# Kernel tuning notes

Hardware: AMD Instinct MI355X
Metric: run time of the kernel (lower is better)

The kernel has to match this reference:

```python
import jax, jax.numpy as jnp
import numpy as np

N = 100000
E = 1600000
IN_DIM = 128
HID = 64


def setup_inputs() -> dict:
    key = jax.random.key(0)
    ks = jax.random.split(key, 10)
    x = jax.random.normal(ks[0], (N, IN_DIM), dtype=jnp.float32)
    edge_index = jax.random.randint(ks[1], (2, E), 0, N, dtype=jnp.int32)
    s1 = 1.0 / np.sqrt(IN_DIM)
    s2 = 1.0 / np.sqrt(HID)
    return {
        "x": x,
        "edge_index": edge_index,
        "W1_l": jax.random.uniform(ks[2], (IN_DIM, HID), jnp.float32, -s1, s1),
        "W1_r": jax.random.uniform(ks[3], (IN_DIM, HID), jnp.float32, -s1, s1),
        "b1": jnp.zeros((HID,), jnp.float32),
        "W2_l": jax.random.uniform(ks[4], (HID, HID), jnp.float32, -s2, s2),
        "W2_r": jax.random.uniform(ks[5], (HID, HID), jnp.float32, -s2, s2),
        "b2": jnp.zeros((HID,), jnp.float32),
        "Wc": jax.random.uniform(ks[6], (HID, 1), jnp.float32, -s2, s2),
        "bc": jnp.zeros((1,), jnp.float32),
    }


def _sage_conv(x, src, dst, inv_deg, W_l, W_r, b):
    # mean-aggregate neighbor features: gather x[src], scatter-sum into dst
    msg = x[src]  # [E, d] irregular gather
    agg = jax.ops.segment_sum(msg, dst, num_segments=N) * inv_deg  # [N, d]
    return agg @ W_l + x @ W_r + b


def reference(x, edge_index, W1_l, W1_r, b1, W2_l, W2_r, b2, Wc, bc):
    src, dst = edge_index[0], edge_index[1]
    deg = jax.ops.segment_sum(jnp.ones((E,), jnp.float32), dst, num_segments=N)
    inv_deg = (1.0 / jnp.maximum(deg, 1.0))[:, None]  # [N,1]
    h = jax.nn.relu(_sage_conv(x, src, dst, inv_deg, W1_l, W1_r, b1))
    # dropout is identity at inference
    h = jax.nn.relu(_sage_conv(h, src, dst, inv_deg, W2_l, W2_r, b2))
    return h @ Wc + bc  # [N, 1] raw logits
```

## Files before the change

### kernel.cpp

```cpp
#include <hip/hip_runtime.h>
#include <hip/hip_bf16.h>

#define N_NODES 100000
#define N_EDGES 1600000
#define IN_DIM  128
#define HID     64

#define PSTRIDE 48
#define NBKT      391
#define BCAP2     4608
#define PREA_BLKS 400
#define EPBA      (N_EDGES / PREA_BLKS)
#define PREP_BLKS 12
#define PRE_BLKS  (PREA_BLKS + PREP_BLKS)
#define GEMM1_BLKS 782

typedef __attribute__((ext_vector_type(8))) short bf16x8;
typedef __attribute__((ext_vector_type(4))) float f32x4;
typedef __attribute__((ext_vector_type(8))) float f32x8;
typedef __attribute__((ext_vector_type(2))) float f32x2;
typedef __attribute__((ext_vector_type(4))) int   i32x4;

__device__ inline unsigned short f2bf_u(float x) {
    __hip_bfloat16 h = __float2bfloat16(x);
    return __builtin_bit_cast(unsigned short, h);
}
__device__ inline float bfu2f(unsigned short u) {
    unsigned v = ((unsigned)u) << 16;
    return __builtin_bit_cast(float, v);
}
__device__ inline unsigned char f2fp8(float x) {
    unsigned e = (unsigned)__builtin_amdgcn_cvt_pk_fp8_f32(x, x, 0, false);
    return (unsigned char)(e & 0xff);
}
__device__ inline void acc_fp8x8(f32x8& acc, uint2 m) {
    f32x2 p0 = __builtin_amdgcn_cvt_pk_f32_fp8(m.x, false);
    f32x2 p1 = __builtin_amdgcn_cvt_pk_f32_fp8(m.x, true);
    f32x2 p2 = __builtin_amdgcn_cvt_pk_f32_fp8(m.y, false);
    f32x2 p3 = __builtin_amdgcn_cvt_pk_f32_fp8(m.y, true);
    acc[0] += p0[0]; acc[1] += p0[1];
    acc[2] += p1[0]; acc[3] += p1[1];
    acc[4] += p2[0]; acc[5] += p2[1];
    acc[6] += p3[0]; acc[7] += p3[1];
}
__device__ inline void acc_bf16x8(f32x8& acc, bf16x8 m) {
#pragma unroll
    for (int q = 0; q < 8; ++q) acc[q] += bfu2f((unsigned short)m[q]);
}

__device__ inline void prep_pack(const float* __restrict__ Wl,
                                 const float* __restrict__ Wr,
                                 ushort2* __restrict__ Bhi,
                                 ushort2* __restrict__ Blo, int idx) {
    int j  = idx & 3;
    int l  = (idx >> 2) & 63;
    int c  = (idx >> 8) & 7;
    int kt = idx >> 11;
    int col = c * 16 + (l & 15);
    int k0  = kt * 32 + (l >> 4) * 8 + 2 * j;
    const float* W = (col < 64) ? Wl : Wr;
    int cc = col & 63;
    float w0 = W[(size_t)k0 * 64 + cc];
    float w1 = W[(size_t)(k0 + 1) * 64 + cc];
    unsigned short h0 = f2bf_u(w0), h1 = f2bf_u(w1);
    unsigned short lo0 = f2bf_u(w0 - bfu2f(h0)), lo1 = f2bf_u(w1 - bfu2f(h1));
    Bhi[idx] = make_ushort2(h0, h1);
    Blo[idx] = make_ushort2(lo0, lo1);
}

__global__ __launch_bounds__(1024) void k_pre(const int* __restrict__ ei,
                                              int* __restrict__ gcnt,
                                              uint2* __restrict__ ebuf,
                                              const float* __restrict__ W1l,
                                              const float* __restrict__ W1r,
                                              const float* __restrict__ W2l,
                                              const float* __restrict__ W2r,
                                              ushort2* __restrict__ Bh1,
                                              ushort2* __restrict__ Bl1,
                                              ushort2* __restrict__ Bh2,
                                              ushort2* __restrict__ Bl2) {
    const int tid = threadIdx.x;
    if (blockIdx.x >= PREA_BLKS) {
        int idx = (blockIdx.x - PREA_BLKS) * 1024 + tid;
        if (idx < 8192)       prep_pack(W1l, W1r, Bh1, Bl1, idx);
        else if (idx < 12288) prep_pack(W2l, W2r, Bh2, Bl2, idx - 8192);
        return;
    }
    __shared__ int hist[NBKT], gbase[NBKT];
    for (int i = tid; i < NBKT; i += 1024) hist[i] = 0;
    __syncthreads();
    const int start = blockIdx.x * EPBA;
    const int end   = start + EPBA;
    const int* __restrict__ src = ei;
    const int* __restrict__ dst = ei + N_EDGES;
    for (int i = start + tid; i < end; i += 1024)
        atomicAdd(&hist[dst[i] >> 8], 1);
    __syncthreads();
    for (int i = tid; i < NBKT; i += 1024) {
        int h = hist[i];
        gbase[i] = (h > 0) ? atomicAdd(&gcnt[i], h) : 0;
        hist[i] = 0;
    }
    __syncthreads();
    for (int i = start + tid; i < end; i += 1024) {
        int d = dst[i];
        int s = src[i];
        int b = d >> 8;
        int r = gbase[b] + atomicAdd(&hist[b], 1);
        if (r < BCAP2) ebuf[(size_t)b * BCAP2 + r] = make_uint2((unsigned)d, (unsigned)s);
    }
}

__global__ __launch_bounds__(256) void k_preB(const int* __restrict__ gcnt,
                                              const uint2* __restrict__ ebuf,
                                              int* __restrict__ adj,
                                              int* __restrict__ deg) {
    __shared__ int adjL[256 * PSTRIDE];
    __shared__ int degL[256];
    const int b   = blockIdx.x;
    const int tid = threadIdx.x;
    degL[tid] = 0;
    {
        i32x4* z4 = (i32x4*)adjL;
        for (int i = tid; i < 256 * PSTRIDE / 4; i += 256) z4[i] = (i32x4)(0);
    }
    __syncthreads();
    const int cnt  = min(gcnt[b], BCAP2);
    const int base = b << 8;
    const uint2* __restrict__ eb = ebuf + (size_t)b * BCAP2;
    for (int i = tid; i < cnt; i += 256) {
        uint2 p = eb[i];
        int r = (int)p.x - base;
        int pos = atomicAdd(&degL[r], 1);
        if (pos < PSTRIDE) adjL[r * PSTRIDE + pos] = (int)p.y;
    }
    __syncthreads();
    const int node = base + tid;
    if (node < N_NODES) deg[node] = degL[tid];
    i32x4* __restrict__ dstp = (i32x4*)(adj + (size_t)base * PSTRIDE);
    const i32x4* __restrict__ srcp = (const i32x4*)adjL;
    for (int i = tid; i < 256 * PSTRIDE / 4; i += 256)
        dstp[i] = srcp[i];
}

__global__ __launch_bounds__(256) void k_gemm1(const float* __restrict__ X,
                                               const i32x4* __restrict__ Bhi,
                                               const i32x4* __restrict__ Blo,
                                               const float* __restrict__ bias,
                                               unsigned char* __restrict__ Yf8,
                                               unsigned short* __restrict__ Dbf, int n) {
    const int K = IN_DIM;
    const int lane = threadIdx.x & 63;
    const int wid  = threadIdx.x >> 6;
    const int m0   = (blockIdx.x * 4 + wid) * 32;
    if (m0 >= n) return;
    const int r  = lane & 15;
    const int kg = lane >> 4;

    f32x4 acc[2][8];
#pragma unroll
    for (int mt = 0; mt < 2; ++mt)
#pragma unroll
        for (int c = 0; c < 8; ++c) acc[mt][c] = (f32x4)(0.f);

#pragma unroll
    for (int kt = 0; kt < K / 32; ++kt) {
        bf16x8 ah[2];
#pragma unroll
        for (int mt = 0; mt < 2; ++mt) {
            const f32x4* p = (const f32x4*)(X + (size_t)(m0 + mt * 16 + r) * K + kt * 32 + kg * 8);
            f32x4 x0 = __builtin_nontemporal_load(p);
            f32x4 x1 = __builtin_nontemporal_load(p + 1);
#pragma unroll
            for (int t = 0; t < 4; ++t) {
                ah[mt][t]     = (short)f2bf_u(x0[t]);
                ah[mt][4 + t] = (short)f2bf_u(x1[t]);
            }
        }
#pragma unroll
        for (int c = 0; c < 8; ++c) {
            const int bi = (kt * 8 + c) * 64 + lane;
            bf16x8 bh = __builtin_bit_cast(bf16x8, Bhi[bi]);
            bf16x8 bl = __builtin_bit_cast(bf16x8, Blo[bi]);
#pragma unroll
            for (int mt = 0; mt < 2; ++mt) {
                acc[mt][c] = __builtin_amdgcn_mfma_f32_16x16x32_bf16(ah[mt], bh, acc[mt][c], 0, 0, 0);
                acc[mt][c] = __builtin_amdgcn_mfma_f32_16x16x32_bf16(ah[mt], bl, acc[mt][c], 0, 0, 0);
            }
        }
    }
#pragma unroll
    for (int mt = 0; mt < 2; ++mt) {
#pragma unroll
        for (int c = 0; c < 8; ++c) {
            int col = c * 16 + r;
            float badd = (c >= 4) ? bias[col - 64] : 0.f;
#pragma unroll
            for (int j = 0; j < 4; ++j) {
                int row = m0 + mt * 16 + kg * 4 + j;
                if (row < n) {
                    if (c < 4) Yf8[(size_t)row * 64 + col] = f2fp8(acc[mt][c][j]);
                    else       Dbf[(size_t)row * 64 + col - 64] = f2bf_u(acc[mt][c][j] + badd);
                }
            }
        }
    }
}

__global__ __launch_bounds__(256) void k_agg1f(const unsigned char* __restrict__ Af8,
                                               unsigned short* __restrict__ Dbf,
                                               const int* __restrict__ adj,
                                               const int* __restrict__ deg,
                                               const i32x4* __restrict__ Bhi,
                                               const i32x4* __restrict__ Blo,
                                               const float* __restrict__ bias,
                                               unsigned short* __restrict__ Bbf) {
    __shared__ unsigned short hs[32][72];
    __shared__ int adjL[32][PSTRIDE];
    __shared__ int degL[32];
    const int tid  = threadIdx.x;
    const int lane = tid & 63;
    const int wv   = tid >> 6;
    const int v0   = blockIdx.x * 32;
    {
        const int* asrc = adj + (size_t)v0 * PSTRIDE;
        for (int i = tid; i < 32 * PSTRIDE; i += 256) ((int*)adjL)[i] = asrc[i];
        if (tid < 32) degL[tid] = deg[v0 + tid];
    }
    __syncthreads();
    const int t  = lane >> 3;
    const int c  = lane & 7;
    const int nt = wv * 8 + t;
    const int v  = v0 + nt;
    const int dgf = degL[nt];
    const int d = min(dgf, PSTRIDE);
    const float iv = 1.0f / (float)max(dgf, 1);
    const uint2* __restrict__ A2 = (const uint2*)Af8;
    f32x8 acc = (f32x8)(0.f);
    int i = 0;
    for (; i + 4 <= d; i += 4) {
        int u0 = adjL[nt][i], u1 = adjL[nt][i + 1], u2 = adjL[nt][i + 2], u3 = adjL[nt][i + 3];
        uint2 m0 = A2[(size_t)u0 * 8 + c];
        uint2 m1 = A2[(size_t)u1 * 8 + c];
        uint2 m2 = A2[(size_t)u2 * 8 + c];
        uint2 m3 = A2[(size_t)u3 * 8 + c];
        acc_fp8x8(acc, m0); acc_fp8x8(acc, m1); acc_fp8x8(acc, m2); acc_fp8x8(acc, m3);
    }
    for (; i < d; ++i) {
        int u0 = adjL[nt][i];
        uint2 m0 = A2[(size_t)u0 * 8 + c];
        acc_fp8x8(acc, m0);
    }
    {
        bf16x8 zb = ((const bf16x8*)Dbf)[(size_t)v * 8 + c];
        bf16x8 hb;
#pragma unroll
        for (int q = 0; q < 8; ++q)
            hb[q] = (short)f2bf_u(fmaxf(fmaf(acc[q], iv, bfu2f((unsigned short)zb[q])), 0.f));
        *(bf16x8*)&hs[nt][c * 8] = hb;
    }
    __syncthreads();
    const int r  = lane & 15;
    const int kg = lane >> 4;
    f32x4 acc2[2][2];
#pragma unroll
    for (int mt = 0; mt < 2; ++mt)
#pragma unroll
        for (int ci = 0; ci < 2; ++ci) acc2[mt][ci] = (f32x4)(0.f);
#pragma unroll
    for (int kt = 0; kt < 2; ++kt) {
        bf16x8 ah[2];
#pragma unroll
        for (int mt = 0; mt < 2; ++mt)
            ah[mt] = *(const bf16x8*)&hs[mt * 16 + r][kt * 32 + kg * 8];
#pragma unroll
        for (int ci = 0; ci < 2; ++ci) {
            const int cg = wv * 2 + ci;
            const int bi = (kt * 8 + cg) * 64 + lane;
            bf16x8 bh = __builtin_bit_cast(bf16x8, Bhi[bi]);
            bf16x8 bl = __builtin_bit_cast(bf16x8, Blo[bi]);
#pragma unroll
            for (int mt = 0; mt < 2; ++mt) {
                acc2[mt][ci] = __builtin_amdgcn_mfma_f32_16x16x32_bf16(ah[mt], bh, acc2[mt][ci], 0, 0, 0);
                acc2[mt][ci] = __builtin_amdgcn_mfma_f32_16x16x32_bf16(ah[mt], bl, acc2[mt][ci], 0, 0, 0);
            }
        }
    }
#pragma unroll
    for (int mt = 0; mt < 2; ++mt) {
#pragma unroll
        for (int ci = 0; ci < 2; ++ci) {
            const int cg = wv * 2 + ci;
            const int col = cg * 16 + r;
            const float badd = (cg >= 4) ? bias[col - 64] : 0.f;
#pragma unroll
            for (int jj = 0; jj < 4; ++jj) {
                const int row = v0 + mt * 16 + kg * 4 + jj;
                if (cg < 4) Bbf[(size_t)row * 64 + col] = f2bf_u(acc2[mt][ci][jj]);
                else        Dbf[(size_t)row * 64 + col - 64] = f2bf_u(acc2[mt][ci][jj] + badd);
            }
        }
    }
}

__global__ __launch_bounds__(256) void k_agg2(const unsigned short* __restrict__ Abf,
                                              const unsigned short* __restrict__ Zbf,
                                              const int* __restrict__ adj,
                                              const int* __restrict__ deg,
                                              const float* __restrict__ Wc,
                                              const float* __restrict__ bc,
                                              float* __restrict__ out, int n) {
    __shared__ int adjL[32][PSTRIDE];
    __shared__ int degL[32];
    const int tid  = threadIdx.x;
    const int lane = tid & 63;
    const int wv   = tid >> 6;
    const int v0   = blockIdx.x * 32;
    {
        const int* asrc = adj + (size_t)v0 * PSTRIDE;
        for (int i = tid; i < 32 * PSTRIDE; i += 256) ((int*)adjL)[i] = asrc[i];
        if (tid < 32) degL[tid] = deg[v0 + tid];
    }
    __syncthreads();
    const int t  = lane >> 3;
    const int c  = lane & 7;
    const int nt = wv * 8 + t;
    const int v  = v0 + nt;
    const int dgf = degL[nt];
    const int d = min(dgf, PSTRIDE);
    const float iv = 1.0f / (float)max(dgf, 1);
    const bf16x8* __restrict__ A8 = (const bf16x8*)Abf;
    f32x8 acc = (f32x8)(0.f);
    int i = 0;
    for (; i + 4 <= d; i += 4) {
        int u0 = adjL[nt][i], u1 = adjL[nt][i + 1], u2 = adjL[nt][i + 2], u3 = adjL[nt][i + 3];
        bf16x8 m0 = A8[(size_t)u0 * 8 + c];
        bf16x8 m1 = A8[(size_t)u1 * 8 + c];
        bf16x8 m2 = A8[(size_t)u2 * 8 + c];
        bf16x8 m3 = A8[(size_t)u3 * 8 + c];
        acc_bf16x8(acc, m0); acc_bf16x8(acc, m1); acc_bf16x8(acc, m2); acc_bf16x8(acc, m3);
    }
    for (; i < d; ++i) {
        int u0 = adjL[nt][i];
        bf16x8 m0 = A8[(size_t)u0 * 8 + c];
        acc_bf16x8(acc, m0);
    }
    bf16x8 zb = ((const bf16x8*)Zbf)[(size_t)v * 8 + c];
    const float4* Wc4 = (const float4*)Wc;
    float4 w0 = Wc4[c * 2], w1 = Wc4[c * 2 + 1];
    float h;
    float pv = 0.f;
    h = fmaxf(fmaf(acc[0], iv, bfu2f((unsigned short)zb[0])), 0.f); pv += h * w0.x;
    h = fmaxf(fmaf(acc[1], iv, bfu2f((unsigned short)zb[1])), 0.f); pv += h * w0.y;
    h = fmaxf(fmaf(acc[2], iv, bfu2f((unsigned short)zb[2])), 0.f); pv += h * w0.z;
    h = fmaxf(fmaf(acc[3], iv, bfu2f((unsigned short)zb[3])), 0.f); pv += h * w0.w;
    h = fmaxf(fmaf(acc[4], iv, bfu2f((unsigned short)zb[4])), 0.f); pv += h * w1.x;
    h = fmaxf(fmaf(acc[5], iv, bfu2f((unsigned short)zb[5])), 0.f); pv += h * w1.y;
    h = fmaxf(fmaf(acc[6], iv, bfu2f((unsigned short)zb[6])), 0.f); pv += h * w1.z;
    h = fmaxf(fmaf(acc[7], iv, bfu2f((unsigned short)zb[7])), 0.f); pv += h * w1.w;
    pv += __shfl_xor(pv, 1, 64);
    pv += __shfl_xor(pv, 2, 64);
    pv += __shfl_xor(pv, 4, 64);
    if (c == 0 && v < n) out[v] = pv + bc[0];
}

extern "C" void kernel_launch(void* const* d_in, const int* in_sizes, int n_in,
                              void* d_out, int out_size, void* d_ws, size_t ws_size,
                              hipStream_t stream) {
    const float* x   = (const float*)d_in[0];
    const int*   ei  = (const int*)d_in[1];
    const float* W1l = (const float*)d_in[2];
    const float* W1r = (const float*)d_in[3];
    const float* b1  = (const float*)d_in[4];
    const float* W2l = (const float*)d_in[5];
    const float* W2r = (const float*)d_in[6];
    const float* b2  = (const float*)d_in[7];
    const float* Wc  = (const float*)d_in[8];
    const float* bc  = (const float*)d_in[9];
    float* out = (float*)d_out;

    char* w = (char*)d_ws;
    auto carve = [&](size_t bytes) -> void* {
        void* p = (void*)w;
        w += (bytes + 255) & ~(size_t)255;
        return p;
    };
    int* gcnt = (int*)carve((size_t)NBKT * 4);
    int* deg  = (int*)carve((size_t)N_NODES * 4);
    int* adj  = (int*)carve((size_t)(N_NODES + 256) * PSTRIDE * 4);
    unsigned char*  Af8 = (unsigned char*)carve((size_t)N_NODES * HID);
    unsigned short* Bbf = (unsigned short*)carve((size_t)N_NODES * HID * 2);
    unsigned short* Dbf = (unsigned short*)carve((size_t)N_NODES * HID * 2);
    uint2* ebuf = (uint2*)carve((size_t)NBKT * BCAP2 * 8);
    ushort2* Bh1 = (ushort2*)carve((size_t)(IN_DIM / 32) * 8 * 64 * 4 * 4);
    ushort2* Bl1 = (ushort2*)carve((size_t)(IN_DIM / 32) * 8 * 64 * 4 * 4);
    ushort2* Bh2 = (ushort2*)carve((size_t)(HID / 32) * 8 * 64 * 4 * 4);
    ushort2* Bl2 = (ushort2*)carve((size_t)(HID / 32) * 8 * 64 * 4 * 4);

    hipMemsetAsync(gcnt, 0, (size_t)NBKT * 4, stream);

    k_pre<<<PRE_BLKS, 1024, 0, stream>>>(ei, gcnt, ebuf, W1l, W1r, W2l, W2r, Bh1, Bl1, Bh2, Bl2);
    k_preB<<<NBKT, 256, 0, stream>>>(gcnt, ebuf, adj, deg);
    k_gemm1<<<GEMM1_BLKS, 256, 0, stream>>>(x, (const i32x4*)Bh1, (const i32x4*)Bl1, b1, Af8, Dbf, N_NODES);
    k_agg1f<<<N_NODES / 32, 256, 0, stream>>>(Af8, Dbf, adj, deg,
                                              (const i32x4*)Bh2, (const i32x4*)Bl2, b2, Bbf);
    k_agg2<<<N_NODES / 32, 256, 0, stream>>>(Bbf, Dbf, adj, deg, Wc, bc, out, N_NODES);
}
```

Measured before the change: 136.8 us.

## Store layer-2 gather table as fp8 and unroll neighbor gathers by eight

The layer-2 projected neighbor features written by the first aggregation kernel are now stored as fp8 instead of bf16, and the second aggregation gathers them with fp8 unpacking. This halves the bytes moved by the irregular per-edge gather. Both aggregation loops also issue eight independent gathers per iteration to raise memory-level parallelism. The shared adjacency tile is padded to 49 ints per row to avoid LDS bank conflicts. The fp8 storage adds quantization error to the second layer's aggregated messages.

```diff
diff --git a/kernel.cpp b/kernel.cpp
--- a/kernel.cpp
+++ b/kernel.cpp
@@ -7,6 +7,7 @@
 #define HID     64
 
 #define PSTRIDE 48
+#define PADJ    49
 #define NBKT      391
 #define BCAP2     4608
 #define PREA_BLKS 400
@@ -42,10 +43,6 @@
     acc[2] += p1[0]; acc[3] += p1[1];
     acc[4] += p2[0]; acc[5] += p2[1];
     acc[6] += p3[0]; acc[7] += p3[1];
-}
-__device__ inline void acc_bf16x8(f32x8& acc, bf16x8 m) {
-#pragma unroll
-    for (int q = 0; q < 8; ++q) acc[q] += bfu2f((unsigned short)m[q]);
 }
 
 __device__ inline void prep_pack(const float* __restrict__ Wl,
@@ -214,9 +211,9 @@
                                                const i32x4* __restrict__ Bhi,
                                                const i32x4* __restrict__ Blo,
                                                const float* __restrict__ bias,
-                                               unsigned short* __restrict__ Bbf) {
+                                               unsigned char* __restrict__ Bf8) {
     __shared__ unsigned short hs[32][72];
-    __shared__ int adjL[32][PSTRIDE];
+    __shared__ int adjL[32][PADJ];
     __shared__ int degL[32];
     const int tid  = threadIdx.x;
     const int lane = tid & 63;
@@ -224,7 +221,8 @@
     const int v0   = blockIdx.x * 32;
     {
         const int* asrc = adj + (size_t)v0 * PSTRIDE;
-        for (int i = tid; i < 32 * PSTRIDE; i += 256) ((int*)adjL)[i] = asrc[i];
+        for (int i = tid; i < 32 * PSTRIDE; i += 256)
+            adjL[i / PSTRIDE][i % PSTRIDE] = asrc[i];
         if (tid < 32) degL[tid] = deg[v0 + tid];
     }
     __syncthreads();
@@ -238,6 +236,20 @@
     const uint2* __restrict__ A2 = (const uint2*)Af8;
     f32x8 acc = (f32x8)(0.f);
     int i = 0;
+    for (; i + 8 <= d; i += 8) {
+        int u0 = adjL[nt][i],     u1 = adjL[nt][i + 1], u2 = adjL[nt][i + 2], u3 = adjL[nt][i + 3];
+        int u4 = adjL[nt][i + 4], u5 = adjL[nt][i + 5], u6 = adjL[nt][i + 6], u7 = adjL[nt][i + 7];
+        uint2 m0 = A2[(size_t)u0 * 8 + c];
+        uint2 m1 = A2[(size_t)u1 * 8 + c];
+        uint2 m2 = A2[(size_t)u2 * 8 + c];
+        uint2 m3 = A2[(size_t)u3 * 8 + c];
+        uint2 m4 = A2[(size_t)u4 * 8 + c];
+        uint2 m5 = A2[(size_t)u5 * 8 + c];
+        uint2 m6 = A2[(size_t)u6 * 8 + c];
+        uint2 m7 = A2[(size_t)u7 * 8 + c];
+        acc_fp8x8(acc, m0); acc_fp8x8(acc, m1); acc_fp8x8(acc, m2); acc_fp8x8(acc, m3);
+        acc_fp8x8(acc, m4); acc_fp8x8(acc, m5); acc_fp8x8(acc, m6); acc_fp8x8(acc, m7);
+    }
     for (; i + 4 <= d; i += 4) {
         int u0 = adjL[nt][i], u1 = adjL[nt][i + 1], u2 = adjL[nt][i + 2], u3 = adjL[nt][i + 3];
         uint2 m0 = A2[(size_t)u0 * 8 + c];
@@ -247,8 +259,7 @@
         acc_fp8x8(acc, m0); acc_fp8x8(acc, m1); acc_fp8x8(acc, m2); acc_fp8x8(acc, m3);
     }
     for (; i < d; ++i) {
-        int u0 = adjL[nt][i];
-        uint2 m0 = A2[(size_t)u0 * 8 + c];
+        uint2 m0 = A2[(size_t)adjL[nt][i] * 8 + c];
         acc_fp8x8(acc, m0);
     }
     {
@@ -296,21 +307,21 @@
 #pragma unroll
             for (int jj = 0; jj < 4; ++jj) {
                 const int row = v0 + mt * 16 + kg * 4 + jj;
-                if (cg < 4) Bbf[(size_t)row * 64 + col] = f2bf_u(acc2[mt][ci][jj]);
+                if (cg < 4) Bf8[(size_t)row * 64 + col] = f2fp8(acc2[mt][ci][jj]);
                 else        Dbf[(size_t)row * 64 + col - 64] = f2bf_u(acc2[mt][ci][jj] + badd);
             }
         }
     }
 }
 
-__global__ __launch_bounds__(256) void k_agg2(const unsigned short* __restrict__ Abf,
+__global__ __launch_bounds__(256) void k_agg2(const unsigned char* __restrict__ Bf8,
                                               const unsigned short* __restrict__ Zbf,
                                               const int* __restrict__ adj,
                                               const int* __restrict__ deg,
                                               const float* __restrict__ Wc,
                                               const float* __restrict__ bc,
                                               float* __restrict__ out, int n) {
-    __shared__ int adjL[32][PSTRIDE];
+    __shared__ int adjL[32][PADJ];
     __shared__ int degL[32];
     const int tid  = threadIdx.x;
     const int lane = tid & 63;
@@ -318,7 +329,8 @@
     const int v0   = blockIdx.x * 32;
     {
         const int* asrc = adj + (size_t)v0 * PSTRIDE;
-        for (int i = tid; i < 32 * PSTRIDE; i += 256) ((int*)adjL)[i] = asrc[i];
+        for (int i = tid; i < 32 * PSTRIDE; i += 256)
+            adjL[i / PSTRIDE][i % PSTRIDE] = asrc[i];
         if (tid < 32) degL[tid] = deg[v0 + tid];
     }
     __syncthreads();
@@ -329,21 +341,34 @@
     const int dgf = degL[nt];
     const int d = min(dgf, PSTRIDE);
     const float iv = 1.0f / (float)max(dgf, 1);
-    const bf16x8* __restrict__ A8 = (const bf16x8*)Abf;
+    const uint2* __restrict__ A2 = (const uint2*)Bf8;
     f32x8 acc = (f32x8)(0.f);
     int i = 0;
+    for (; i + 8 <= d; i += 8) {
+        int u0 = adjL[nt][i],     u1 = adjL[nt][i + 1], u2 = adjL[nt][i + 2], u3 = adjL[nt][i + 3];
+        int u4 = adjL[nt][i + 4], u5 = adjL[nt][i + 5], u6 = adjL[nt][i + 6], u7 = adjL[nt][i + 7];
+        uint2 m0 = A2[(size_t)u0 * 8 + c];
+        uint2 m1 = A2[(size_t)u1 * 8 + c];
+        uint2 m2 = A2[(size_t)u2 * 8 + c];
+        uint2 m3 = A2[(size_t)u3 * 8 + c];
+        uint2 m4 = A2[(size_t)u4 * 8 + c];
+        uint2 m5 = A2[(size_t)u5 * 8 + c];
+        uint2 m6 = A2[(size_t)u6 * 8 + c];
+        uint2 m7 = A2[(size_t)u7 * 8 + c];
+        acc_fp8x8(acc, m0); acc_fp8x8(acc, m1); acc_fp8x8(acc, m2); acc_fp8x8(acc, m3);
+        acc_fp8x8(acc, m4); acc_fp8x8(acc, m5); acc_fp8x8(acc, m6); acc_fp8x8(acc, m7);
+    }
     for (; i + 4 <= d; i += 4) {
         int u0 = adjL[nt][i], u1 = adjL[nt][i + 1], u2 = adjL[nt][i + 2], u3 = adjL[nt][i + 3];
-        bf16x8 m0 = A8[(size_t)u0 * 8 + c];
-        bf16x8 m1 = A8[(size_t)u1 * 8 + c];
-        bf16x8 m2 = A8[(size_t)u2 * 8 + c];
-        bf16x8 m3 = A8[(size_t)u3 * 8 + c];
-        acc_bf16x8(acc, m0); acc_bf16x8(acc, m1); acc_bf16x8(acc, m2); acc_bf16x8(acc, m3);
+        uint2 m0 = A2[(size_t)u0 * 8 + c];
+        uint2 m1 = A2[(size_t)u1 * 8 + c];
+        uint2 m2 = A2[(size_t)u2 * 8 + c];
+        uint2 m3 = A2[(size_t)u3 * 8 + c];
+        acc_fp8x8(acc, m0); acc_fp8x8(acc, m1); acc_fp8x8(acc, m2); acc_fp8x8(acc, m3);
     }
     for (; i < d; ++i) {
-        int u0 = adjL[nt][i];
-        bf16x8 m0 = A8[(size_t)u0 * 8 + c];
-        acc_bf16x8(acc, m0);
+        uint2 m0 = A2[(size_t)adjL[nt][i] * 8 + c];
+        acc_fp8x8(acc, m0);
     }
     bf16x8 zb = ((const bf16x8*)Zbf)[(size_t)v * 8 + c];
     const float4* Wc4 = (const float4*)Wc;
@@ -389,7 +414,7 @@
     int* deg  = (int*)carve((size_t)N_NODES * 4);
     int* adj  = (int*)carve((size_t)(N_NODES + 256) * PSTRIDE * 4);
     unsigned char*  Af8 = (unsigned char*)carve((size_t)N_NODES * HID);
-    unsigned short* Bbf = (unsigned short*)carve((size_t)N_NODES * HID * 2);
+    unsigned char*  Bf8 = (unsigned char*)carve((size_t)N_NODES * HID);
     unsigned short* Dbf = (unsigned short*)carve((size_t)N_NODES * HID * 2);
     uint2* ebuf = (uint2*)carve((size_t)NBKT * BCAP2 * 8);
     ushort2* Bh1 = (ushort2*)carve((size_t)(IN_DIM / 32) * 8 * 64 * 4 * 4);
@@ -403,6 +428,6 @@
     k_preB<<<NBKT, 256, 0, stream>>>(gcnt, ebuf, adj, deg);
     k_gemm1<<<GEMM1_BLKS, 256, 0, stream>>>(x, (const i32x4*)Bh1, (const i32x4*)Bl1, b1, Af8, Dbf, N_NODES);
     k_agg1f<<<N_NODES / 32, 256, 0, stream>>>(Af8, Dbf, adj, deg,
-                                              (const i32x4*)Bh2, (const i32x4*)Bl2, b2, Bbf);
-    k_agg2<<<N_NODES / 32, 256, 0, stream>>>(Bbf, Dbf, adj, deg, Wc, bc, out, N_NODES);
-}
+                                              (const i32x4*)Bh2, (const i32x4*)Bl2, b2, Bf8);
+    k_agg2<<<N_NODES / 32, 256, 0, stream>>>(Bf8, Dbf, adj, deg, Wc, bc, out, N_NODES);
+}
```

Result: faster. 130.1 us (-4.9%).
